# Kernel tuning notes

Measured on AMD Instinct MI355X. Metric: run time of the kernel, lower is better.

Reference implementation:

```python
import jax, jax.numpy as jnp
import numpy as np

B, H, S, D = 4, 16, 2048, 128
D_MODEL = 128  # scale factor per module init


def setup_inputs() -> dict:
    key = jax.random.key(0)
    kq, kk, kv = jax.random.split(key, 3)
    Q = jax.random.normal(kq, (B, H, S, D), dtype=jnp.float32)
    K = jax.random.normal(kk, (B, H, S, D), dtype=jnp.float32)
    V = jax.random.normal(kv, (B, H, S, D), dtype=jnp.float32)
    return {"Q": Q, "K": K, "V": V}


def reference(Q, K, V):
    # scores: [B, H, S, S]
    scores = jnp.einsum("bhqd,bhkd->bhqk", Q, K) / np.sqrt(D_MODEL).astype(np.float32)
    # causal mask: lower-triangular keeps, upper becomes -inf
    q_idx = jnp.arange(S)[:, None]
    k_idx = jnp.arange(S)[None, :]
    causal = q_idx >= k_idx  # [S, S]
    scores = jnp.where(causal, scores, -jnp.inf)
    attn = jax.nn.softmax(scores, axis=-1)
    return jnp.einsum("bhqk,bhkd->bhqd", attn, V)
```

## Files before the change

### kernel.cpp

```cpp
#include <hip/hip_runtime.h>

typedef _Float16 f16;
typedef _Float16 f16x8 __attribute__((ext_vector_type(8)));
typedef float    f32x16 __attribute__((ext_vector_type(16)));
typedef int      i32x4 __attribute__((ext_vector_type(4)));

#define B_ 4
#define H_ 16
#define S_ 2048
#define D_ 128
#define KVB 32
#define KSTR 136
#define VTSTR 40

union U4 { i32x4 i; f16x8 h; };

__device__ __forceinline__ unsigned pk2(float a, float b) {
    auto v = __builtin_amdgcn_cvt_pkrtz(a, b);
    return __builtin_bit_cast(unsigned, v);
}

__device__ __forceinline__ f16x8 cvt8(const float4 a, const float4 b) {
    f16x8 h;
    h[0] = (f16)a.x; h[1] = (f16)a.y; h[2] = (f16)a.z; h[3] = (f16)a.w;
    h[4] = (f16)b.x; h[5] = (f16)b.y; h[6] = (f16)b.z; h[7] = (f16)b.w;
    return h;
}

__global__ __launch_bounds__(256)
void prep(const float* __restrict__ K, const float* __restrict__ V,
          f16* __restrict__ Kh, f16* __restrict__ Vtt)
{
    const int bid = blockIdx.x;
    const int bh  = bid >> 5;
    const int kb  = bid & 31;
    const int k0  = kb * 64;
    const int tid = threadIdx.x;

    const float* Kb = K + ((size_t)bh * S_ + k0) * D_;
    const float* Vb = V + ((size_t)bh * S_ + k0) * D_;
    f16* Khb = Kh + ((size_t)bh * S_ + k0) * D_;
    f16* Vtb = Vtt + (size_t)bh * S_ * D_ + (size_t)kb * 2 * (D_ * 32);

    #pragma unroll
    for (int it = 0; it < 4; ++it) {
        const int idx = tid + it * 256;
        const int row = idx >> 4, c8 = idx & 15;
        const float4 a = *(const float4*)(Kb + row * D_ + c8 * 8);
        const float4 b = *(const float4*)(Kb + row * D_ + c8 * 8 + 4);
        *(f16x8*)(Khb + row * D_ + c8 * 8) = cvt8(a, b);
    }
    #pragma unroll
    for (int it = 0; it < 4; ++it) {
        const int idx = tid + it * 256;
        const int d  = idx & 127;
        const int k8 = idx >> 7;
        const int t  = k8 >> 2;
        const int o  = k8 & 3;
        const int c  = o >> 1, odd = o & 1;
        const int kbase = t * 32 + c * 16 + odd * 4;
        const float* vp0 = Vb + (size_t)kbase * D_ + d;
        const float* vp1 = vp0 + (size_t)8 * D_;
        f16x8 vh;
        #pragma unroll
        for (int e = 0; e < 4; ++e) vh[e] = (f16)vp0[(size_t)e * D_];
        #pragma unroll
        for (int e = 0; e < 4; ++e) vh[4 + e] = (f16)vp1[(size_t)e * D_];
        *(f16x8*)(Vtb + (size_t)t * (D_ * 32) + d * 32 + o * 8) = vh;
    }
}

__global__ __launch_bounds__(256, 2)
void fattn15(const float* __restrict__ Qg, const f16* __restrict__ Khg,
             const f16* __restrict__ Vttg, float* __restrict__ Og)
{
    __shared__ __align__(16) f16 Klds[4][KVB * KSTR];
    __shared__ __align__(16) f16 Vt[4][128 * VTSTR];

    const int id  = blockIdx.x;
    const int xcd = id & 7;
    const int r   = id >> 3;
    const int bh  = xcd + 8 * (r & 7);
    const int p   = r >> 3;

    const int tid  = threadIdx.x;
    const int lane = tid & 63;
    const int l31  = lane & 31;
    const int h    = lane >> 5;
    const int wv   = tid >> 6;

    const float* Qb  = Qg   + (size_t)bh * S_ * D_;
    const f16*   Khb = Khg  + (size_t)bh * S_ * D_;
    const f16*   Vtb = Vttg + (size_t)bh * S_ * D_;
    float*       Ob  = Og   + (size_t)bh * S_ * D_;

    const f16* kS = Khb + (tid >> 4) * D_ + (tid & 15) * 8;
    const f16* vS = Vtb + (size_t)tid * 8;
    const int  kDo = (tid >> 4) * KSTR + (tid & 15) * 8;
    const int  vDo = (tid >> 2) * VTSTR + (tid & 3) * 8;

    i32x4 kr[2], vr[2];
    auto issue = [&](int kt) {
        const f16* kp = kS + ((size_t)kt << 12);
        const f16* vp = vS + ((size_t)kt << 12);
        kr[0] = *(const i32x4*)kp;
        kr[1] = *(const i32x4*)(kp + 2048);
        vr[0] = *(const i32x4*)vp;
        vr[1] = *(const i32x4*)(vp + 2048);
    };
    auto writeLds = [&](int buf) {
        f16* kb = &Klds[buf][0];
        f16* vb = &Vt[buf][0];
        *(i32x4*)(kb + kDo)              = kr[0];
        *(i32x4*)(kb + kDo + 16 * KSTR)  = kr[1];
        *(i32x4*)(vb + vDo)              = vr[0];
        *(i32x4*)(vb + vDo + 64 * VTSTR) = vr[1];
    };
    f16x8 qf[8];
    auto qkt = [&](int buf) {
        f32x16 a;
        #pragma unroll
        for (int rr = 0; rr < 16; ++rr) a[rr] = 0.f;
        #pragma unroll
        for (int dc = 0; dc < 8; ++dc) {
            const f16x8 kf = *(const f16x8*)&Klds[buf][l31 * KSTR + dc * 16 + h * 8];
            a = __builtin_amdgcn_mfma_f32_32x32x16_f16(kf, qf[dc], a, 0, 0, 0);
        }
        return a;
    };

    const float qmul = 0.08838834764831845f * 1.4426950408889634f;

    #pragma unroll 1
    for (int ph = 0; ph < 2; ++ph) {
        const int qt  = ph ? 15 - p : p;
        const int qw0 = qt * 128 + wv * 32;
        const int qg  = qw0 + l31;
        const int nkt = 4 * qt + 4;
        const int lastt = 4 * qt + wv;

        {
            const float* Qrow = Qb + (size_t)(qw0 + l31) * D_;
            #pragma unroll
            for (int dc = 0; dc < 8; ++dc) {
                const float4 a = *(const float4*)(Qrow + dc * 16 + h * 8);
                const float4 b = *(const float4*)(Qrow + dc * 16 + h * 8 + 4);
                f16x8 q;
                q[0] = (f16)(a.x * qmul); q[1] = (f16)(a.y * qmul);
                q[2] = (f16)(a.z * qmul); q[3] = (f16)(a.w * qmul);
                q[4] = (f16)(b.x * qmul); q[5] = (f16)(b.y * qmul);
                q[6] = (f16)(b.z * qmul); q[7] = (f16)(b.w * qmul);
                qf[dc] = q;
            }
        }

        f32x16 acc[4];
        #pragma unroll
        for (int dt = 0; dt < 4; ++dt)
            #pragma unroll
            for (int rr = 0; rr < 16; ++rr) acc[dt][rr] = 0.f;
        float m_i = -1e30f, l_i = 0.f;

        __syncthreads();
        issue(0);  writeLds(0);
        issue(1);  writeLds(1);
        if (nkt > 2) issue(2);
        __syncthreads();
        f32x16 sv = qkt(0);

        U4 pa0c, pa1c, pa0p, pa1p;

        for (int kt = 0; kt < nkt; ++kt) {
            __syncthreads();
            if (kt + 2 < nkt) {
                writeLds((kt + 2) & 3);
                if (kt + 3 < nkt) issue(kt + 3);
            }

            __builtin_amdgcn_s_setprio(1);
            f32x16 svn;
            const bool doA = (kt + 1 < nkt) && (kt + 1 <= lastt);
            if (doA) svn = qkt((kt + 1) & 3);

            if (kt >= 1 && kt - 1 <= lastt) {
                const f16* vbase = &Vt[(kt - 1) & 3][l31 * VTSTR + h * 8];
                #pragma unroll
                for (int dt = 0; dt < 4; ++dt) {
                    const f16x8 vb0 = *(const f16x8*)(vbase + dt * 32 * VTSTR);
                    const f16x8 vb1 = *(const f16x8*)(vbase + dt * 32 * VTSTR + 16);
                    acc[dt] = __builtin_amdgcn_mfma_f32_32x32x16_f16(pa0p.h, vb0, acc[dt], 0, 0, 0);
                    acc[dt] = __builtin_amdgcn_mfma_f32_32x32x16_f16(pa1p.h, vb1, acc[dt], 0, 0, 0);
                }
            }

            if (kt <= lastt) {
                const int k0 = kt * KVB;
                if (k0 + 31 > qw0) {
                    #pragma unroll
                    for (int rr = 0; rr < 16; ++rr) {
                        const int kg = k0 + (rr & 3) + 8 * (rr >> 2) + 4 * h;
                        if (kg > qg) sv[rr] = -1e30f;
                    }
                }
                const float m1 = fmaxf(fmaxf(sv[0], sv[1]), sv[2]);
                const float m2 = fmaxf(fmaxf(sv[3], sv[4]), sv[5]);
                const float m3 = fmaxf(fmaxf(sv[6], sv[7]), sv[8]);
                const float m4 = fmaxf(fmaxf(sv[9], sv[10]), sv[11]);
                const float m5 = fmaxf(fmaxf(sv[12], sv[13]), sv[14]);
                float mx = fmaxf(fmaxf(m1, m2), m3);
                mx = fmaxf(fmaxf(mx, m4), m5);
                mx = fmaxf(mx, sv[15]);
                mx = fmaxf(mx, __shfl_xor(mx, 32));
                if (!__all(mx - m_i <= 8.0f)) {
                    const float mn = fmaxf(m_i, mx);
                    const float al = exp2f(m_i - mn);
                    m_i = mn;
                    l_i *= al;
                    float arow[16];
                    #pragma unroll
                    for (int rr = 0; rr < 16; ++rr)
                        arow[rr] = __shfl(al, (rr & 3) + 8 * (rr >> 2) + 4 * h);
                    #pragma unroll
                    for (int dt = 0; dt < 4; ++dt)
                        #pragma unroll
                        for (int rr = 0; rr < 16; ++rr) acc[dt][rr] *= arow[rr];
                }
                #pragma unroll
                for (int rr = 0; rr < 16; ++rr) sv[rr] = exp2f(sv[rr] - m_i);
                float s8[8];
                #pragma unroll
                for (int rr = 0; rr < 8; ++rr) s8[rr] = sv[2 * rr] + sv[2 * rr + 1];
                #pragma unroll
                for (int rr = 0; rr < 4; ++rr) s8[rr] += s8[rr + 4];
                s8[0] += s8[2]; s8[1] += s8[3];
                float rs = s8[0] + s8[1];
                rs += __shfl_xor(rs, 32);
                l_i += rs;
                #pragma unroll
                for (int m = 0; m < 4; ++m) pa0c.i[m] = (int)pk2(sv[2 * m],     sv[2 * m + 1]);
                #pragma unroll
                for (int m = 0; m < 4; ++m) pa1c.i[m] = (int)pk2(sv[8 + 2 * m], sv[9 + 2 * m]);
            }
            __builtin_amdgcn_s_setprio(0);

            pa0p = pa0c; pa1p = pa1c;
            if (doA) sv = svn;
        }

        if (lastt == nkt - 1) {
            const f16* vbase = &Vt[lastt & 3][l31 * VTSTR + h * 8];
            #pragma unroll
            for (int dt = 0; dt < 4; ++dt) {
                const f16x8 vb0 = *(const f16x8*)(vbase + dt * 32 * VTSTR);
                const f16x8 vb1 = *(const f16x8*)(vbase + dt * 32 * VTSTR + 16);
                acc[dt] = __builtin_amdgcn_mfma_f32_32x32x16_f16(pa0p.h, vb0, acc[dt], 0, 0, 0);
                acc[dt] = __builtin_amdgcn_mfma_f32_32x32x16_f16(pa1p.h, vb1, acc[dt], 0, 0, 0);
            }
        }

        float li[16];
        #pragma unroll
        for (int rr = 0; rr < 16; ++rr) {
            const float lv = __shfl(l_i, (rr & 3) + 8 * (rr >> 2) + 4 * h);
            li[rr] = 1.0f / lv;
        }
        #pragma unroll
        for (int dt = 0; dt < 4; ++dt)
            #pragma unroll
            for (int rr = 0; rr < 16; ++rr) {
                const int row = qw0 + (rr & 3) + 8 * (rr >> 2) + 4 * h;
                Ob[(size_t)row * D_ + dt * 32 + l31] = acc[dt][rr] * li[rr];
            }
    }
}

__global__ __launch_bounds__(256, 3)
void fattn5(const float* __restrict__ Qg, const float* __restrict__ Kg,
            const float* __restrict__ Vg, float* __restrict__ Og)
{
    __shared__ __align__(16) f16 Klds[2][KVB * KSTR];
    __shared__ __align__(16) f16 Vt[2][128 * VTSTR];
    const int id  = blockIdx.x;
    const int xcd = id & 7;
    const int w   = id >> 3;
    const int qt  = 15 - (w & 15);
    const int bh  = xcd + 8 * (w >> 4);
    const int tid  = threadIdx.x;
    const int lane = tid & 63;
    const int wv   = tid >> 6;
    const int l31  = lane & 31;
    const int h    = lane >> 5;
    const int qw0 = qt * 128 + wv * 32;
    const int qg  = qw0 + l31;
    const size_t base = (size_t)bh * S_ * D_;
    const float* Qb = Qg + base;
    const float* Kb = Kg + base;
    const float* Vb = Vg + base;
    float*       Ob = Og + base;
    const int nkt = 4 * qt + 4;
    float4 kr[4];
    float  vr[16];
    auto issue = [&](int kt) {
        const int k0n = kt * KVB;
        #pragma unroll
        for (int it = 0; it < 2; ++it) {
            const int idx  = tid + it * 256;
            const int krow = idx >> 4;
            const int c8   = idx & 15;
            const float* kp = Kb + (size_t)(k0n + krow) * D_ + c8 * 8;
            kr[it * 2]     = *(const float4*)kp;
            kr[it * 2 + 1] = *(const float4*)(kp + 4);
            const int d  = idx & 127;
            const int k8 = idx >> 7;
            const float* vp = Vb + (size_t)(k0n + k8 * 8) * D_ + d;
            #pragma unroll
            for (int e = 0; e < 8; ++e) vr[it * 8 + e] = vp[(size_t)e * D_];
        }
    };
    auto writeLds = [&](int buf) {
        #pragma unroll
        for (int it = 0; it < 2; ++it) {
            const int idx  = tid + it * 256;
            const int krow = idx >> 4;
            const int c8   = idx & 15;
            *(f16x8*)&Klds[buf][krow * KSTR + c8 * 8] = cvt8(kr[it * 2], kr[it * 2 + 1]);
            const int d  = idx & 127;
            const int k8 = idx >> 7;
            f16x8 vh;
            #pragma unroll
            for (int e = 0; e < 8; ++e) vh[e] = (f16)vr[it * 8 + e];
            *(f16x8*)&Vt[buf][d * VTSTR + k8 * 8] = vh;
        }
    };
    const float qmul = 0.08838834764831845f * 1.4426950408889634f;
    f16x8 qf[8];
    {
        const float* Qrow = Qb + (size_t)(qw0 + l31) * D_;
        #pragma unroll
        for (int dc = 0; dc < 8; ++dc) {
            const float4 a = *(const float4*)(Qrow + dc * 16 + h * 8);
            const float4 b = *(const float4*)(Qrow + dc * 16 + h * 8 + 4);
            f16x8 q;
            q[0] = (f16)(a.x * qmul); q[1] = (f16)(a.y * qmul);
            q[2] = (f16)(a.z * qmul); q[3] = (f16)(a.w * qmul);
            q[4] = (f16)(b.x * qmul); q[5] = (f16)(b.y * qmul);
            q[6] = (f16)(b.z * qmul); q[7] = (f16)(b.w * qmul);
            qf[dc] = q;
        }
    }
    f32x16 acc[4];
    #pragma unroll
    for (int dt = 0; dt < 4; ++dt)
        #pragma unroll
        for (int rr = 0; rr < 16; ++rr) acc[dt][rr] = 0.f;
    float m_i = -1e30f, l_i = 0.f;
    issue(0);
    writeLds(0);
    if (nkt > 1) issue(1);
    __syncthreads();
    for (int kt = 0; kt < nkt; ++kt) {
        const int k0  = kt * KVB;
        const int cur = kt & 1;
        if (k0 <= qw0 + 31) {
            f32x16 sv;
            #pragma unroll
            for (int rr = 0; rr < 16; ++rr) sv[rr] = 0.f;
            #pragma unroll
            for (int dc = 0; dc < 8; ++dc) {
                const f16x8 kf = *(const f16x8*)&Klds[cur][l31 * KSTR + dc * 16 + h * 8];
                sv = __builtin_amdgcn_mfma_f32_32x32x16_f16(kf, qf[dc], sv, 0, 0, 0);
            }
            if (k0 + 31 > qw0) {
                #pragma unroll
                for (int rr = 0; rr < 16; ++rr) {
                    const int kg = k0 + (rr & 3) + 8 * (rr >> 2) + 4 * h;
                    if (kg > qg) sv[rr] = -1e30f;
                }
            }
            float mx = sv[0];
            #pragma unroll
            for (int rr = 1; rr < 16; ++rr) mx = fmaxf(mx, sv[rr]);
            mx = fmaxf(mx, __shfl_xor(mx, 32));
            if (!__all(mx - m_i <= 8.0f)) {
                const float mn = fmaxf(m_i, mx);
                const float al = exp2f(m_i - mn);
                m_i = mn;
                l_i *= al;
                float arow[16];
                #pragma unroll
                for (int rr = 0; rr < 16; ++rr)
                    arow[rr] = __shfl(al, (rr & 3) + 8 * (rr >> 2) + 4 * h);
                #pragma unroll
                for (int dt = 0; dt < 4; ++dt)
                    #pragma unroll
                    for (int rr = 0; rr < 16; ++rr) acc[dt][rr] *= arow[rr];
            }
            float rs = 0.f;
            #pragma unroll
            for (int rr = 0; rr < 16; ++rr) {
                sv[rr] = exp2f(sv[rr] - m_i);
                rs += sv[rr];
            }
            rs += __shfl_xor(rs, 32);
            l_i += rs;
            U4 pa[2];
            {
                unsigned dwp[8];
                #pragma unroll
                for (int m = 0; m < 8; ++m) dwp[m] = pk2(sv[2 * m], sv[2 * m + 1]);
                #pragma unroll
                for (int hf = 0; hf < 2; ++hf) {
                    const unsigned a0 = dwp[hf * 4 + 0], a1 = dwp[hf * 4 + 1];
                    const unsigned b0 = dwp[hf * 4 + 2], b1 = dwp[hf * 4 + 3];
                    const unsigned sa0 = (unsigned)__shfl_xor((int)a0, 32);
                    const unsigned sa1 = (unsigned)__shfl_xor((int)a1, 32);
                    const unsigned sb0 = (unsigned)__shfl_xor((int)b0, 32);
                    const unsigned sb1 = (unsigned)__shfl_xor((int)b1, 32);
                    i32x4 d;
                    d[0] = h ? (int)sb0 : (int)a0;
                    d[1] = h ? (int)sb1 : (int)a1;
                    d[2] = h ? (int)b0  : (int)sa0;
                    d[3] = h ? (int)b1  : (int)sa1;
                    pa[hf].i = d;
                }
            }
            #pragma unroll
            for (int dt = 0; dt < 4; ++dt) {
                const f16* vrow = &Vt[cur][(dt * 32 + l31) * VTSTR + h * 8];
                const f16x8 vb0 = *(const f16x8*)(vrow + 0);
                const f16x8 vb1 = *(const f16x8*)(vrow + 16);
                acc[dt] = __builtin_amdgcn_mfma_f32_32x32x16_f16(pa[0].h, vb0, acc[dt], 0, 0, 0);
                acc[dt] = __builtin_amdgcn_mfma_f32_32x32x16_f16(pa[1].h, vb1, acc[dt], 0, 0, 0);
            }
        }
        if (kt + 1 < nkt) {
            writeLds(cur ^ 1);
            if (kt + 2 < nkt) issue(kt + 2);
            __syncthreads();
        }
    }
    float li[16];
    #pragma unroll
    for (int rr = 0; rr < 16; ++rr) {
        const float lv = __shfl(l_i, (rr & 3) + 8 * (rr >> 2) + 4 * h);
        li[rr] = 1.0f / lv;
    }
    #pragma unroll
    for (int dt = 0; dt < 4; ++dt)
        #pragma unroll
        for (int rr = 0; rr < 16; ++rr) {
            const int row = qw0 + (rr & 3) + 8 * (rr >> 2) + 4 * h;
            Ob[(size_t)row * D_ + dt * 32 + l31] = acc[dt][rr] * li[rr];
        }
}

extern "C" void kernel_launch(void* const* d_in, const int* in_sizes, int n_in,
                              void* d_out, int out_size, void* d_ws, size_t ws_size,
                              hipStream_t stream) {
    (void)in_sizes; (void)n_in; (void)out_size;
    const float* Q = (const float*)d_in[0];
    const float* K = (const float*)d_in[1];
    const float* V = (const float*)d_in[2];
    float* O = (float*)d_out;
    const size_t elems  = (size_t)B_ * H_ * S_ * D_;
    const size_t needKV = elems * 2 * sizeof(f16);
    if (ws_size >= needKV) {
        f16* Kh  = (f16*)d_ws;
        f16* Vtt = Kh + elems;
        prep<<<dim3(B_ * H_ * (S_ / 64)), dim3(256), 0, stream>>>(K, V, Kh, Vtt);
        fattn15<<<dim3(512), dim3(256), 0, stream>>>(Q, Kh, Vtt, O);
    } else {
        fattn5<<<dim3((S_ / 128) * B_ * H_), dim3(256), 0, stream>>>(Q, K, V, O);
    }
}
```

Measured before the change: 156.0 us.

## Use 64-key tiles with double buffering instead of 4-stage software-pipelined 32-key tiles

Doubles the KV tile to 64 keys and drops from four LDS buffers to two. It also removes the software pipelining that overlapped the next tile's QK^T with the current PV, and instead computes two 32-key score blocks per iteration in sequence. This halves the number of barriers and iterations and raises MFMA work per sync. In exchange it loses the cross-iteration overlap and coarsens causal skipping, so wasted masked work grows on diagonal tiles.

Result: no change. 156.3 us (+0.2%).

```diff
diff --git a/kernel.cpp b/kernel.cpp
--- a/kernel.cpp
+++ b/kernel.cpp
@@ -9,9 +9,9 @@
 #define H_ 16
 #define S_ 2048
 #define D_ 128
-#define KVB 32
+#define KVB 64
 #define KSTR 136
-#define VTSTR 40
+#define VT2  72
 
 union U4 { i32x4 i; f16x8 h; };
 
@@ -71,11 +71,11 @@
 }
 
 __global__ __launch_bounds__(256, 2)
-void fattn15(const float* __restrict__ Qg, const f16* __restrict__ Khg,
+void fattn16(const float* __restrict__ Qg, const f16* __restrict__ Khg,
              const f16* __restrict__ Vttg, float* __restrict__ Og)
 {
-    __shared__ __align__(16) f16 Klds[4][KVB * KSTR];
-    __shared__ __align__(16) f16 Vt[4][128 * VTSTR];
+    __shared__ __align__(16) f16 Klds[2][KVB * KSTR];
+    __shared__ __align__(16) f16 Vl[2][128 * VT2];
 
     const int id  = blockIdx.x;
     const int xcd = id & 7;
@@ -97,37 +97,31 @@
     const f16* kS = Khb + (tid >> 4) * D_ + (tid & 15) * 8;
     const f16* vS = Vtb + (size_t)tid * 8;
     const int  kDo = (tid >> 4) * KSTR + (tid & 15) * 8;
-    const int  vDo = (tid >> 2) * VTSTR + (tid & 3) * 8;
-
-    i32x4 kr[2], vr[2];
+    const int  vDo = (tid >> 2) * VT2 + (tid & 3) * 8;
+
+    i32x4 kr[4], vr[4];
     auto issue = [&](int kt) {
-        const f16* kp = kS + ((size_t)kt << 12);
-        const f16* vp = vS + ((size_t)kt << 12);
-        kr[0] = *(const i32x4*)kp;
-        kr[1] = *(const i32x4*)(kp + 2048);
-        vr[0] = *(const i32x4*)vp;
-        vr[1] = *(const i32x4*)(vp + 2048);
+        const f16* kp = kS + ((size_t)kt << 13);
+        const f16* vp = vS + ((size_t)kt << 13);
+        #pragma unroll
+        for (int it = 0; it < 4; ++it) {
+            kr[it] = *(const i32x4*)(kp + it * 2048);
+            vr[it] = *(const i32x4*)(vp + it * 2048);
+        }
     };
     auto writeLds = [&](int buf) {
         f16* kb = &Klds[buf][0];
-        f16* vb = &Vt[buf][0];
+        f16* vb = &Vl[buf][0];
         *(i32x4*)(kb + kDo)              = kr[0];
         *(i32x4*)(kb + kDo + 16 * KSTR)  = kr[1];
+        *(i32x4*)(kb + kDo + 32 * KSTR)  = kr[2];
+        *(i32x4*)(kb + kDo + 48 * KSTR)  = kr[3];
         *(i32x4*)(vb + vDo)              = vr[0];
-        *(i32x4*)(vb + vDo + 64 * VTSTR) = vr[1];
+        *(i32x4*)(vb + vDo + 64 * VT2)   = vr[1];
+        *(i32x4*)(vb + vDo + 32)         = vr[2];
+        *(i32x4*)(vb + vDo + 64 * VT2 + 32) = vr[3];
     };
     f16x8 qf[8];
-    auto qkt = [&](int buf) {
-        f32x16 a;
-        #pragma unroll
-        for (int rr = 0; rr < 16; ++rr) a[rr] = 0.f;
-        #pragma unroll
-        for (int dc = 0; dc < 8; ++dc) {
-            const f16x8 kf = *(const f16x8*)&Klds[buf][l31 * KSTR + dc * 16 + h * 8];
-            a = __builtin_amdgcn_mfma_f32_32x32x16_f16(kf, qf[dc], a, 0, 0, 0);
-        }
-        return a;
-    };
 
     const float qmul = 0.08838834764831845f * 1.4426950408889634f;
 
@@ -136,9 +130,10 @@
         const int qt  = ph ? 15 - p : p;
         const int qw0 = qt * 128 + wv * 32;
         const int qg  = qw0 + l31;
-        const int nkt = 4 * qt + 4;
-        const int lastt = 4 * qt + wv;
-
+        const int nt  = 2 * qt + 2;
+        const int lastt = (4 * qt + wv) >> 1;
+
+        issue(0);
         {
             const float* Qrow = Qb + (size_t)(qw0 + l31) * D_;
             #pragma unroll
@@ -162,54 +157,43 @@
         float m_i = -1e30f, l_i = 0.f;
 
         __syncthreads();
-        issue(0);  writeLds(0);
-        issue(1);  writeLds(1);
-        if (nkt > 2) issue(2);
+        writeLds(0);
+        if (nt > 1) issue(1);
         __syncthreads();
-        f32x16 sv = qkt(0);
-
-        U4 pa0c, pa1c, pa0p, pa1p;
-
-        for (int kt = 0; kt < nkt; ++kt) {
-            __syncthreads();
-            if (kt + 2 < nkt) {
-                writeLds((kt + 2) & 3);
-                if (kt + 3 < nkt) issue(kt + 3);
-            }
-
-            __builtin_amdgcn_s_setprio(1);
-            f32x16 svn;
-            const bool doA = (kt + 1 < nkt) && (kt + 1 <= lastt);
-            if (doA) svn = qkt((kt + 1) & 3);
-
-            if (kt >= 1 && kt - 1 <= lastt) {
-                const f16* vbase = &Vt[(kt - 1) & 3][l31 * VTSTR + h * 8];
-                #pragma unroll
-                for (int dt = 0; dt < 4; ++dt) {
-                    const f16x8 vb0 = *(const f16x8*)(vbase + dt * 32 * VTSTR);
-                    const f16x8 vb1 = *(const f16x8*)(vbase + dt * 32 * VTSTR + 16);
-                    acc[dt] = __builtin_amdgcn_mfma_f32_32x32x16_f16(pa0p.h, vb0, acc[dt], 0, 0, 0);
-                    acc[dt] = __builtin_amdgcn_mfma_f32_32x32x16_f16(pa1p.h, vb1, acc[dt], 0, 0, 0);
-                }
-            }
+
+        for (int kt = 0; kt < nt; ++kt) {
+            const int cur = kt & 1;
 
             if (kt <= lastt) {
                 const int k0 = kt * KVB;
-                if (k0 + 31 > qw0) {
+                f32x16 sv0, sv1;
+                #pragma unroll
+                for (int rr = 0; rr < 16; ++rr) { sv0[rr] = 0.f; sv1[rr] = 0.f; }
+                __builtin_amdgcn_s_setprio(1);
+                #pragma unroll
+                for (int dc = 0; dc < 8; ++dc) {
+                    const f16x8 kf0 = *(const f16x8*)&Klds[cur][l31 * KSTR + dc * 16 + h * 8];
+                    const f16x8 kf1 = *(const f16x8*)&Klds[cur][(32 + l31) * KSTR + dc * 16 + h * 8];
+                    sv0 = __builtin_amdgcn_mfma_f32_32x32x16_f16(kf0, qf[dc], sv0, 0, 0, 0);
+                    sv1 = __builtin_amdgcn_mfma_f32_32x32x16_f16(kf1, qf[dc], sv1, 0, 0, 0);
+                }
+                __builtin_amdgcn_s_setprio(0);
+                if (k0 + 63 > qw0) {
                     #pragma unroll
                     for (int rr = 0; rr < 16; ++rr) {
-                        const int kg = k0 + (rr & 3) + 8 * (rr >> 2) + 4 * h;
-                        if (kg > qg) sv[rr] = -1e30f;
+                        const int kk = k0 + (rr & 3) + 8 * (rr >> 2) + 4 * h;
+                        if (kk > qg)      sv0[rr] = -1e30f;
+                        if (kk + 32 > qg) sv1[rr] = -1e30f;
                     }
                 }
-                const float m1 = fmaxf(fmaxf(sv[0], sv[1]), sv[2]);
-                const float m2 = fmaxf(fmaxf(sv[3], sv[4]), sv[5]);
-                const float m3 = fmaxf(fmaxf(sv[6], sv[7]), sv[8]);
-                const float m4 = fmaxf(fmaxf(sv[9], sv[10]), sv[11]);
-                const float m5 = fmaxf(fmaxf(sv[12], sv[13]), sv[14]);
-                float mx = fmaxf(fmaxf(m1, m2), m3);
-                mx = fmaxf(fmaxf(mx, m4), m5);
-                mx = fmaxf(mx, sv[15]);
+                float t16[16];
+                #pragma unroll
+                for (int rr = 0; rr < 16; ++rr) t16[rr] = fmaxf(sv0[rr], sv1[rr]);
+                #pragma unroll
+                for (int rr = 0; rr < 8; ++rr) t16[rr] = fmaxf(t16[rr], t16[rr + 8]);
+                #pragma unroll
+                for (int rr = 0; rr < 4; ++rr) t16[rr] = fmaxf(t16[rr], t16[rr + 4]);
+                float mx = fmaxf(fmaxf(t16[0], t16[1]), fmaxf(t16[2], t16[3]));
                 mx = fmaxf(mx, __shfl_xor(mx, 32));
                 if (!__all(mx - m_i <= 8.0f)) {
                     const float mn = fmaxf(m_i, mx);
@@ -226,35 +210,48 @@
                         for (int rr = 0; rr < 16; ++rr) acc[dt][rr] *= arow[rr];
                 }
                 #pragma unroll
-                for (int rr = 0; rr < 16; ++rr) sv[rr] = exp2f(sv[rr] - m_i);
-                float s8[8];
-                #pragma unroll
-                for (int rr = 0; rr < 8; ++rr) s8[rr] = sv[2 * rr] + sv[2 * rr + 1];
-                #pragma unroll
-                for (int rr = 0; rr < 4; ++rr) s8[rr] += s8[rr + 4];
-                s8[0] += s8[2]; s8[1] += s8[3];
-                float rs = s8[0] + s8[1];
+                for (int rr = 0; rr < 16; ++rr) {
+                    sv0[rr] = exp2f(sv0[rr] - m_i);
+                    sv1[rr] = exp2f(sv1[rr] - m_i);
+                }
+                float s16[16];
+                #pragma unroll
+                for (int rr = 0; rr < 16; ++rr) s16[rr] = sv0[rr] + sv1[rr];
+                #pragma unroll
+                for (int rr = 0; rr < 8; ++rr) s16[rr] += s16[rr + 8];
+                #pragma unroll
+                for (int rr = 0; rr < 4; ++rr) s16[rr] += s16[rr + 4];
+                float rs = (s16[0] + s16[1]) + (s16[2] + s16[3]);
                 rs += __shfl_xor(rs, 32);
                 l_i += rs;
-                #pragma unroll
-                for (int m = 0; m < 4; ++m) pa0c.i[m] = (int)pk2(sv[2 * m],     sv[2 * m + 1]);
-                #pragma unroll
-                for (int m = 0; m < 4; ++m) pa1c.i[m] = (int)pk2(sv[8 + 2 * m], sv[9 + 2 * m]);
-            }
-            __builtin_amdgcn_s_setprio(0);
-
-            pa0p = pa0c; pa1p = pa1c;
-            if (doA) sv = svn;
-        }
-
-        if (lastt == nkt - 1) {
-            const f16* vbase = &Vt[lastt & 3][l31 * VTSTR + h * 8];
-            #pragma unroll
-            for (int dt = 0; dt < 4; ++dt) {
-                const f16x8 vb0 = *(const f16x8*)(vbase + dt * 32 * VTSTR);
-                const f16x8 vb1 = *(const f16x8*)(vbase + dt * 32 * VTSTR + 16);
-                acc[dt] = __builtin_amdgcn_mfma_f32_32x32x16_f16(pa0p.h, vb0, acc[dt], 0, 0, 0);
-                acc[dt] = __builtin_amdgcn_mfma_f32_32x32x16_f16(pa1p.h, vb1, acc[dt], 0, 0, 0);
+                U4 pa[4];
+                #pragma unroll
+                for (int m = 0; m < 4; ++m) {
+                    pa[0].i[m] = (int)pk2(sv0[2 * m],     sv0[2 * m + 1]);
+                    pa[1].i[m] = (int)pk2(sv0[8 + 2 * m], sv0[9 + 2 * m]);
+                    pa[2].i[m] = (int)pk2(sv1[2 * m],     sv1[2 * m + 1]);
+                    pa[3].i[m] = (int)pk2(sv1[8 + 2 * m], sv1[9 + 2 * m]);
+                }
+                __builtin_amdgcn_s_setprio(1);
+                #pragma unroll
+                for (int dt = 0; dt < 4; ++dt) {
+                    const f16* vrow = &Vl[cur][(dt * 32 + l31) * VT2 + h * 8];
+                    const f16x8 b0 = *(const f16x8*)(vrow + 0);
+                    const f16x8 b1 = *(const f16x8*)(vrow + 16);
+                    const f16x8 b2 = *(const f16x8*)(vrow + 32);
+                    const f16x8 b3 = *(const f16x8*)(vrow + 48);
+                    acc[dt] = __builtin_amdgcn_mfma_f32_32x32x16_f16(pa[0].h, b0, acc[dt], 0, 0, 0);
+                    acc[dt] = __builtin_amdgcn_mfma_f32_32x32x16_f16(pa[1].h, b1, acc[dt], 0, 0, 0);
+                    acc[dt] = __builtin_amdgcn_mfma_f32_32x32x16_f16(pa[2].h, b2, acc[dt], 0, 0, 0);
+                    acc[dt] = __builtin_amdgcn_mfma_f32_32x32x16_f16(pa[3].h, b3, acc[dt], 0, 0, 0);
+                }
+                __builtin_amdgcn_s_setprio(0);
+            }
+
+            if (kt + 1 < nt) {
+                writeLds(cur ^ 1);
+                if (kt + 2 < nt) issue(kt + 2);
+                __syncthreads();
             }
         }
 
@@ -274,12 +271,14 @@
     }
 }
 
+#define KVB5 32
+#define VTSTR5 40
 __global__ __launch_bounds__(256, 3)
 void fattn5(const float* __restrict__ Qg, const float* __restrict__ Kg,
             const float* __restrict__ Vg, float* __restrict__ Og)
 {
-    __shared__ __align__(16) f16 Klds[2][KVB * KSTR];
-    __shared__ __align__(16) f16 Vt[2][128 * VTSTR];
+    __shared__ __align__(16) f16 Klds[2][KVB5 * KSTR];
+    __shared__ __align__(16) f16 Vt[2][128 * VTSTR5];
     const int id  = blockIdx.x;
     const int xcd = id & 7;
     const int w   = id >> 3;
@@ -301,7 +300,7 @@
     float4 kr[4];
     float  vr[16];
     auto issue = [&](int kt) {
-        const int k0n = kt * KVB;
+        const int k0n = kt * KVB5;
         #pragma unroll
         for (int it = 0; it < 2; ++it) {
             const int idx  = tid + it * 256;
@@ -329,7 +328,7 @@
             f16x8 vh;
             #pragma unroll
             for (int e = 0; e < 8; ++e) vh[e] = (f16)vr[it * 8 + e];
-            *(f16x8*)&Vt[buf][d * VTSTR + k8 * 8] = vh;
+            *(f16x8*)&Vt[buf][d * VTSTR5 + k8 * 8] = vh;
         }
     };
     const float qmul = 0.08838834764831845f * 1.4426950408889634f;
@@ -359,7 +358,7 @@
     if (nkt > 1) issue(1);
     __syncthreads();
     for (int kt = 0; kt < nkt; ++kt) {
-        const int k0  = kt * KVB;
+        const int k0  = kt * KVB5;
         const int cur = kt & 1;
         if (k0 <= qw0 + 31) {
             f32x16 sv;
@@ -426,7 +425,7 @@
             }
             #pragma unroll
             for (int dt = 0; dt < 4; ++dt) {
-                const f16* vrow = &Vt[cur][(dt * 32 + l31) * VTSTR + h * 8];
+                const f16* vrow = &Vt[cur][(dt * 32 + l31) * VTSTR5 + h * 8];
                 const f16x8 vb0 = *(const f16x8*)(vrow + 0);
                 const f16x8 vb1 = *(const f16x8*)(vrow + 16);
                 acc[dt] = __builtin_amdgcn_mfma_f32_32x32x16_f16(pa[0].h, vb0, acc[dt], 0, 0, 0);
@@ -468,7 +467,7 @@
         f16* Kh  = (f16*)d_ws;
         f16* Vtt = Kh + elems;
         prep<<<dim3(B_ * H_ * (S_ / 64)), dim3(256), 0, stream>>>(K, V, Kh, Vtt);
-        fattn15<<<dim3(512), dim3(256), 0, stream>>>(Q, Kh, Vtt, O);
+        fattn16<<<dim3(512), dim3(256), 0, stream>>>(Q, Kh, Vtt, O);
     } else {
         fattn5<<<dim3((S_ / 128) * B_ * H_), dim3(256), 0, stream>>>(Q, K, V, O);
     }
```

## Split causal KV range into two halves with partial outputs and merge kernel

Applied to the files above, without the earlier changes.

Replaces the paired-qtile persistent attention kernel with a split-K style design. Each query tile is processed by two blocks covering the lower and upper halves of the causal KV range, which write f16 partial outputs plus per-row (m, l) to workspace; a separate merge kernel combines them. Q is also pre-scaled and converted to f16 in the prep kernel, and LDS buffering drops from four to two stages to allow three blocks per CU. This raises parallelism and occupancy, at the cost of extra global traffic for partials, a third launch, f16 rounding of partial outputs, and loss of the software-pipelined QK/PV overlap.

Measured after the change: 185.7 us. 1.19x slower.

```diff
diff --git a/kernel.cpp b/kernel.cpp
--- a/kernel.cpp
+++ b/kernel.cpp
@@ -1,6 +1,7 @@
 #include <hip/hip_runtime.h>
 
 typedef _Float16 f16;
+typedef _Float16 f16x4 __attribute__((ext_vector_type(4)));
 typedef _Float16 f16x8 __attribute__((ext_vector_type(8)));
 typedef float    f32x16 __attribute__((ext_vector_type(16)));
 typedef int      i32x4 __attribute__((ext_vector_type(4)));
@@ -29,17 +30,21 @@
 
 __global__ __launch_bounds__(256)
 void prep(const float* __restrict__ K, const float* __restrict__ V,
-          f16* __restrict__ Kh, f16* __restrict__ Vtt)
+          const float* __restrict__ Q,
+          f16* __restrict__ Kh, f16* __restrict__ Vtt, f16* __restrict__ Qh)
 {
     const int bid = blockIdx.x;
     const int bh  = bid >> 5;
     const int kb  = bid & 31;
     const int k0  = kb * 64;
     const int tid = threadIdx.x;
+    const float qmul = 0.08838834764831845f * 1.4426950408889634f;
 
     const float* Kb = K + ((size_t)bh * S_ + k0) * D_;
     const float* Vb = V + ((size_t)bh * S_ + k0) * D_;
+    const float* Qb = Q + ((size_t)bh * S_ + k0) * D_;
     f16* Khb = Kh + ((size_t)bh * S_ + k0) * D_;
+    f16* Qhb = Qh + ((size_t)bh * S_ + k0) * D_;
     f16* Vtb = Vtt + (size_t)bh * S_ * D_ + (size_t)kb * 2 * (D_ * 32);
 
     #pragma unroll
@@ -49,6 +54,11 @@
         const float4 a = *(const float4*)(Kb + row * D_ + c8 * 8);
         const float4 b = *(const float4*)(Kb + row * D_ + c8 * 8 + 4);
         *(f16x8*)(Khb + row * D_ + c8 * 8) = cvt8(a, b);
+        float4 qa = *(const float4*)(Qb + row * D_ + c8 * 8);
+        float4 qb = *(const float4*)(Qb + row * D_ + c8 * 8 + 4);
+        qa.x *= qmul; qa.y *= qmul; qa.z *= qmul; qa.w *= qmul;
+        qb.x *= qmul; qb.y *= qmul; qb.z *= qmul; qb.w *= qmul;
+        *(f16x8*)(Qhb + row * D_ + c8 * 8) = cvt8(qa, qb);
     }
     #pragma unroll
     for (int it = 0; it < 4; ++it) {
@@ -70,18 +80,21 @@
     }
 }
 
-__global__ __launch_bounds__(256, 2)
-void fattn15(const float* __restrict__ Qg, const f16* __restrict__ Khg,
-             const f16* __restrict__ Vttg, float* __restrict__ Og)
+__global__ __launch_bounds__(256, 3)
+void fattn17(const f16* __restrict__ Qhg, const f16* __restrict__ Khg,
+             const f16* __restrict__ Vttg,
+             f16* __restrict__ Pg, float2* __restrict__ mlg)
 {
-    __shared__ __align__(16) f16 Klds[4][KVB * KSTR];
-    __shared__ __align__(16) f16 Vt[4][128 * VTSTR];
+    __shared__ __align__(16) f16 Klds[2][KVB * KSTR];
+    __shared__ __align__(16) f16 Vl[2][128 * VTSTR];
 
     const int id  = blockIdx.x;
     const int xcd = id & 7;
     const int r   = id >> 3;
     const int bh  = xcd + 8 * (r & 7);
-    const int p   = r >> 3;
+    const int rr  = r >> 3;
+    const int s   = rr & 1;
+    const int qt  = 15 - (rr >> 1);
 
     const int tid  = threadIdx.x;
     const int lane = tid & 63;
@@ -89,10 +102,19 @@
     const int h    = lane >> 5;
     const int wv   = tid >> 6;
 
-    const float* Qb  = Qg   + (size_t)bh * S_ * D_;
-    const f16*   Khb = Khg  + (size_t)bh * S_ * D_;
-    const f16*   Vtb = Vttg + (size_t)bh * S_ * D_;
-    float*       Ob  = Og   + (size_t)bh * S_ * D_;
+    const int qw0 = qt * 128 + wv * 32;
+    const int qg  = qw0 + l31;
+
+    const f16* Qhb = Qhg + (size_t)bh * S_ * D_;
+    const f16* Khb = Khg + (size_t)bh * S_ * D_;
+    const f16* Vtb = Vttg + (size_t)bh * S_ * D_;
+
+    const int nkt  = 4 * qt + 4;
+    const int half = 2 * qt + 2;
+    const int lo   = s ? half : 0;
+    const int hi   = s ? nkt : half;
+    int lastt = 4 * qt + wv;
+    if (lastt > hi - 1) lastt = hi - 1;
 
     const f16* kS = Khb + (tid >> 4) * D_ + (tid & 15) * 8;
     const f16* vS = Vtb + (size_t)tid * 8;
@@ -110,167 +132,156 @@
     };
     auto writeLds = [&](int buf) {
         f16* kb = &Klds[buf][0];
-        f16* vb = &Vt[buf][0];
+        f16* vb = &Vl[buf][0];
         *(i32x4*)(kb + kDo)              = kr[0];
         *(i32x4*)(kb + kDo + 16 * KSTR)  = kr[1];
         *(i32x4*)(vb + vDo)              = vr[0];
         *(i32x4*)(vb + vDo + 64 * VTSTR) = vr[1];
     };
+
     f16x8 qf[8];
-    auto qkt = [&](int buf) {
-        f32x16 a;
-        #pragma unroll
-        for (int rr = 0; rr < 16; ++rr) a[rr] = 0.f;
-        #pragma unroll
-        for (int dc = 0; dc < 8; ++dc) {
-            const f16x8 kf = *(const f16x8*)&Klds[buf][l31 * KSTR + dc * 16 + h * 8];
-            a = __builtin_amdgcn_mfma_f32_32x32x16_f16(kf, qf[dc], a, 0, 0, 0);
-        }
-        return a;
-    };
-
-    const float qmul = 0.08838834764831845f * 1.4426950408889634f;
-
-    #pragma unroll 1
-    for (int ph = 0; ph < 2; ++ph) {
-        const int qt  = ph ? 15 - p : p;
-        const int qw0 = qt * 128 + wv * 32;
-        const int qg  = qw0 + l31;
-        const int nkt = 4 * qt + 4;
-        const int lastt = 4 * qt + wv;
-
-        {
-            const float* Qrow = Qb + (size_t)(qw0 + l31) * D_;
+    {
+        const f16* Qrow = Qhb + (size_t)(qw0 + l31) * D_;
+        #pragma unroll
+        for (int dc = 0; dc < 8; ++dc)
+            qf[dc] = *(const f16x8*)(Qrow + dc * 16 + h * 8);
+    }
+
+    f32x16 acc[4];
+    #pragma unroll
+    for (int dt = 0; dt < 4; ++dt)
+        #pragma unroll
+        for (int q = 0; q < 16; ++q) acc[dt][q] = 0.f;
+    float m_i = -1e30f, l_i = 0.f;
+
+    issue(lo);
+    writeLds(0);
+    if (lo + 1 < hi) issue(lo + 1);
+    __syncthreads();
+
+    for (int kt = lo; kt < hi; ++kt) {
+        const int cur = (kt - lo) & 1;
+
+        if (kt <= lastt) {
+            const int k0 = kt * KVB;
+            f32x16 sv;
+            #pragma unroll
+            for (int q = 0; q < 16; ++q) sv[q] = 0.f;
+            __builtin_amdgcn_s_setprio(1);
             #pragma unroll
             for (int dc = 0; dc < 8; ++dc) {
-                const float4 a = *(const float4*)(Qrow + dc * 16 + h * 8);
-                const float4 b = *(const float4*)(Qrow + dc * 16 + h * 8 + 4);
-                f16x8 q;
-                q[0] = (f16)(a.x * qmul); q[1] = (f16)(a.y * qmul);
-                q[2] = (f16)(a.z * qmul); q[3] = (f16)(a.w * qmul);
-                q[4] = (f16)(b.x * qmul); q[5] = (f16)(b.y * qmul);
-                q[6] = (f16)(b.z * qmul); q[7] = (f16)(b.w * qmul);
-                qf[dc] = q;
-            }
-        }
-
-        f32x16 acc[4];
-        #pragma unroll
-        for (int dt = 0; dt < 4; ++dt)
-            #pragma unroll
-            for (int rr = 0; rr < 16; ++rr) acc[dt][rr] = 0.f;
-        float m_i = -1e30f, l_i = 0.f;
-
-        __syncthreads();
-        issue(0);  writeLds(0);
-        issue(1);  writeLds(1);
-        if (nkt > 2) issue(2);
-        __syncthreads();
-        f32x16 sv = qkt(0);
-
-        U4 pa0c, pa1c, pa0p, pa1p;
-
-        for (int kt = 0; kt < nkt; ++kt) {
+                const f16x8 kf = *(const f16x8*)&Klds[cur][l31 * KSTR + dc * 16 + h * 8];
+                sv = __builtin_amdgcn_mfma_f32_32x32x16_f16(kf, qf[dc], sv, 0, 0, 0);
+            }
+            __builtin_amdgcn_s_setprio(0);
+            if (k0 + 31 > qw0) {
+                #pragma unroll
+                for (int q = 0; q < 16; ++q) {
+                    const int kg = k0 + (q & 3) + 8 * (q >> 2) + 4 * h;
+                    if (kg > qg) sv[q] = -1e30f;
+                }
+            }
+            const float a1 = fmaxf(fmaxf(sv[0], sv[1]), sv[2]);
+            const float a2 = fmaxf(fmaxf(sv[3], sv[4]), sv[5]);
+            const float a3 = fmaxf(fmaxf(sv[6], sv[7]), sv[8]);
+            const float a4 = fmaxf(fmaxf(sv[9], sv[10]), sv[11]);
+            const float a5 = fmaxf(fmaxf(sv[12], sv[13]), sv[14]);
+            float mx = fmaxf(fmaxf(a1, a2), a3);
+            mx = fmaxf(fmaxf(mx, a4), a5);
+            mx = fmaxf(mx, sv[15]);
+            mx = fmaxf(mx, __shfl_xor(mx, 32));
+            if (!__all(mx - m_i <= 8.0f)) {
+                const float mn = fmaxf(m_i, mx);
+                const float al = exp2f(m_i - mn);
+                m_i = mn;
+                l_i *= al;
+                float arow[16];
+                #pragma unroll
+                for (int q = 0; q < 16; ++q)
+                    arow[q] = __shfl(al, (q & 3) + 8 * (q >> 2) + 4 * h);
+                #pragma unroll
+                for (int dt = 0; dt < 4; ++dt)
+                    #pragma unroll
+                    for (int q = 0; q < 16; ++q) acc[dt][q] *= arow[q];
+            }
+            #pragma unroll
+            for (int q = 0; q < 16; ++q) sv[q] = exp2f(sv[q] - m_i);
+            float s8[8];
+            #pragma unroll
+            for (int q = 0; q < 8; ++q) s8[q] = sv[2 * q] + sv[2 * q + 1];
+            #pragma unroll
+            for (int q = 0; q < 4; ++q) s8[q] += s8[q + 4];
+            s8[0] += s8[2]; s8[1] += s8[3];
+            float rsum = s8[0] + s8[1];
+            rsum += __shfl_xor(rsum, 32);
+            l_i += rsum;
+            U4 pa0, pa1;
+            #pragma unroll
+            for (int m = 0; m < 4; ++m) {
+                pa0.i[m] = (int)pk2(sv[2 * m],     sv[2 * m + 1]);
+                pa1.i[m] = (int)pk2(sv[8 + 2 * m], sv[9 + 2 * m]);
+            }
+            __builtin_amdgcn_s_setprio(1);
+            #pragma unroll
+            for (int dt = 0; dt < 4; ++dt) {
+                const f16* vrow = &Vl[cur][(dt * 32 + l31) * VTSTR + h * 8];
+                const f16x8 b0 = *(const f16x8*)(vrow + 0);
+                const f16x8 b1 = *(const f16x8*)(vrow + 16);
+                acc[dt] = __builtin_amdgcn_mfma_f32_32x32x16_f16(pa0.h, b0, acc[dt], 0, 0, 0);
+                acc[dt] = __builtin_amdgcn_mfma_f32_32x32x16_f16(pa1.h, b1, acc[dt], 0, 0, 0);
+            }
+            __builtin_amdgcn_s_setprio(0);
+        }
+
+        if (kt + 1 < hi) {
+            writeLds(cur ^ 1);
+            if (kt + 2 < hi) issue(kt + 2);
             __syncthreads();
-            if (kt + 2 < nkt) {
-                writeLds((kt + 2) & 3);
-                if (kt + 3 < nkt) issue(kt + 3);
-            }
-
-            __builtin_amdgcn_s_setprio(1);
-            f32x16 svn;
-            const bool doA = (kt + 1 < nkt) && (kt + 1 <= lastt);
-            if (doA) svn = qkt((kt + 1) & 3);
-
-            if (kt >= 1 && kt - 1 <= lastt) {
-                const f16* vbase = &Vt[(kt - 1) & 3][l31 * VTSTR + h * 8];
-                #pragma unroll
-                for (int dt = 0; dt < 4; ++dt) {
-                    const f16x8 vb0 = *(const f16x8*)(vbase + dt * 32 * VTSTR);
-                    const f16x8 vb1 = *(const f16x8*)(vbase + dt * 32 * VTSTR + 16);
-                    acc[dt] = __builtin_amdgcn_mfma_f32_32x32x16_f16(pa0p.h, vb0, acc[dt], 0, 0, 0);
-                    acc[dt] = __builtin_amdgcn_mfma_f32_32x32x16_f16(pa1p.h, vb1, acc[dt], 0, 0, 0);
-                }
-            }
-
-            if (kt <= lastt) {
-                const int k0 = kt * KVB;
-                if (k0 + 31 > qw0) {
-                    #pragma unroll
-                    for (int rr = 0; rr < 16; ++rr) {
-                        const int kg = k0 + (rr & 3) + 8 * (rr >> 2) + 4 * h;
-                        if (kg > qg) sv[rr] = -1e30f;
-                    }
-                }
-                const float m1 = fmaxf(fmaxf(sv[0], sv[1]), sv[2]);
-                const float m2 = fmaxf(fmaxf(sv[3], sv[4]), sv[5]);
-                const float m3 = fmaxf(fmaxf(sv[6], sv[7]), sv[8]);
-                const float m4 = fmaxf(fmaxf(sv[9], sv[10]), sv[11]);
-                const float m5 = fmaxf(fmaxf(sv[12], sv[13]), sv[14]);
-                float mx = fmaxf(fmaxf(m1, m2), m3);
-                mx = fmaxf(fmaxf(mx, m4), m5);
-                mx = fmaxf(mx, sv[15]);
-                mx = fmaxf(mx, __shfl_xor(mx, 32));
-                if (!__all(mx - m_i <= 8.0f)) {
-                    const float mn = fmaxf(m_i, mx);
-                    const float al = exp2f(m_i - mn);
-                    m_i = mn;
-                    l_i *= al;
-                    float arow[16];
-                    #pragma unroll
-                    for (int rr = 0; rr < 16; ++rr)
-                        arow[rr] = __shfl(al, (rr & 3) + 8 * (rr >> 2) + 4 * h);
-                    #pragma unroll
-                    for (int dt = 0; dt < 4; ++dt)
-                        #pragma unroll
-                        for (int rr = 0; rr < 16; ++rr) acc[dt][rr] *= arow[rr];
-                }
-                #pragma unroll
-                for (int rr = 0; rr < 16; ++rr) sv[rr] = exp2f(sv[rr] - m_i);
-                float s8[8];
-                #pragma unroll
-                for (int rr = 0; rr < 8; ++rr) s8[rr] = sv[2 * rr] + sv[2 * rr + 1];
-                #pragma unroll
-                for (int rr = 0; rr < 4; ++rr) s8[rr] += s8[rr + 4];
-                s8[0] += s8[2]; s8[1] += s8[3];
-                float rs = s8[0] + s8[1];
-                rs += __shfl_xor(rs, 32);
-                l_i += rs;
-                #pragma unroll
-                for (int m = 0; m < 4; ++m) pa0c.i[m] = (int)pk2(sv[2 * m],     sv[2 * m + 1]);
-                #pragma unroll
-                for (int m = 0; m < 4; ++m) pa1c.i[m] = (int)pk2(sv[8 + 2 * m], sv[9 + 2 * m]);
-            }
-            __builtin_amdgcn_s_setprio(0);
-
-            pa0p = pa0c; pa1p = pa1c;
-            if (doA) sv = svn;
-        }
-
-        if (lastt == nkt - 1) {
-            const f16* vbase = &Vt[lastt & 3][l31 * VTSTR + h * 8];
-            #pragma unroll
-            for (int dt = 0; dt < 4; ++dt) {
-                const f16x8 vb0 = *(const f16x8*)(vbase + dt * 32 * VTSTR);
-                const f16x8 vb1 = *(const f16x8*)(vbase + dt * 32 * VTSTR + 16);
-                acc[dt] = __builtin_amdgcn_mfma_f32_32x32x16_f16(pa0p.h, vb0, acc[dt], 0, 0, 0);
-                acc[dt] = __builtin_amdgcn_mfma_f32_32x32x16_f16(pa1p.h, vb1, acc[dt], 0, 0, 0);
-            }
-        }
-
-        float li[16];
-        #pragma unroll
-        for (int rr = 0; rr < 16; ++rr) {
-            const float lv = __shfl(l_i, (rr & 3) + 8 * (rr >> 2) + 4 * h);
-            li[rr] = 1.0f / lv;
-        }
-        #pragma unroll
-        for (int dt = 0; dt < 4; ++dt)
-            #pragma unroll
-            for (int rr = 0; rr < 16; ++rr) {
-                const int row = qw0 + (rr & 3) + 8 * (rr >> 2) + 4 * h;
-                Ob[(size_t)row * D_ + dt * 32 + l31] = acc[dt][rr] * li[rr];
-            }
+        }
+    }
+
+    float li[16];
+    #pragma unroll
+    for (int q = 0; q < 16; ++q) {
+        const float lv = __shfl(l_i, (q & 3) + 8 * (q >> 2) + 4 * h);
+        li[q] = (lv > 0.f) ? 1.0f / lv : 0.f;
+    }
+    f16* Pb = Pg + ((size_t)s * (B_ * H_) + bh) * (S_ * D_);
+    #pragma unroll
+    for (int dt = 0; dt < 4; ++dt)
+        #pragma unroll
+        for (int q = 0; q < 16; ++q) {
+            const int row = qw0 + (q & 3) + 8 * (q >> 2) + 4 * h;
+            Pb[(size_t)row * D_ + dt * 32 + l31] = (f16)(acc[dt][q] * li[q]);
+        }
+    if (h == 0)
+        mlg[((size_t)s * (B_ * H_) + bh) * S_ + qw0 + l31] = make_float2(m_i, l_i);
+}
+
+__global__ __launch_bounds__(256)
+void merge(const f16* __restrict__ Pg, const float2* __restrict__ mlg,
+           float* __restrict__ O)
+{
+    const size_t NROW   = (size_t)B_ * H_ * S_;
+    const size_t total4 = NROW * (D_ / 4);
+    const size_t stride = (size_t)gridDim.x * 256;
+    for (size_t i = (size_t)blockIdx.x * 256 + threadIdx.x; i < total4; i += stride) {
+        const size_t row = i >> 5;
+        const float2 a = mlg[row];
+        const float2 b = mlg[NROW + row];
+        const float ms = fmaxf(a.x, b.x);
+        float w0 = exp2f(a.x - ms) * a.y;
+        float w1 = exp2f(b.x - ms) * b.y;
+        const float inv = 1.0f / (w0 + w1);
+        w0 *= inv; w1 *= inv;
+        const f16x4 p0 = *(const f16x4*)(Pg + i * 4);
+        const f16x4 p1 = *(const f16x4*)(Pg + NROW * D_ + i * 4);
+        float4 o;
+        o.x = w0 * (float)p0[0] + w1 * (float)p1[0];
+        o.y = w0 * (float)p0[1] + w1 * (float)p1[1];
+        o.z = w0 * (float)p0[2] + w1 * (float)p1[2];
+        o.w = w0 * (float)p0[3] + w1 * (float)p1[3];
+        *(float4*)(O + i * 4) = o;
     }
 }
 
@@ -352,7 +363,7 @@
     #pragma unroll
     for (int dt = 0; dt < 4; ++dt)
         #pragma unroll
-        for (int rr = 0; rr < 16; ++rr) acc[dt][rr] = 0.f;
+        for (int q = 0; q < 16; ++q) acc[dt][q] = 0.f;
     float m_i = -1e30f, l_i = 0.f;
     issue(0);
     writeLds(0);
@@ -364,7 +375,7 @@
         if (k0 <= qw0 + 31) {
             f32x16 sv;
             #pragma unroll
-            for (int rr = 0; rr < 16; ++rr) sv[rr] = 0.f;
+            for (int q = 0; q < 16; ++q) sv[q] = 0.f;
             #pragma unroll
             for (int dc = 0; dc < 8; ++dc) {
                 const f16x8 kf = *(const f16x8*)&Klds[cur][l31 * KSTR + dc * 16 + h * 8];
@@ -372,14 +383,14 @@
             }
             if (k0 + 31 > qw0) {
                 #pragma unroll
-                for (int rr = 0; rr < 16; ++rr) {
-                    const int kg = k0 + (rr & 3) + 8 * (rr >> 2) + 4 * h;
-                    if (kg > qg) sv[rr] = -1e30f;
+                for (int q = 0; q < 16; ++q) {
+                    const int kg = k0 + (q & 3) + 8 * (q >> 2) + 4 * h;
+                    if (kg > qg) sv[q] = -1e30f;
                 }
             }
             float mx = sv[0];
             #pragma unroll
-            for (int rr = 1; rr < 16; ++rr) mx = fmaxf(mx, sv[rr]);
+            for (int q = 1; q < 16; ++q) mx = fmaxf(mx, sv[q]);
             mx = fmaxf(mx, __shfl_xor(mx, 32));
             if (!__all(mx - m_i <= 8.0f)) {
                 const float mn = fmaxf(m_i, mx);
@@ -388,21 +399,21 @@
                 l_i *= al;
                 float arow[16];
                 #pragma unroll
-                for (int rr = 0; rr < 16; ++rr)
-                    arow[rr] = __shfl(al, (rr & 3) + 8 * (rr >> 2) + 4 * h);
+                for (int q = 0; q < 16; ++q)
+                    arow[q] = __shfl(al, (q & 3) + 8 * (q >> 2) + 4 * h);
                 #pragma unroll
                 for (int dt = 0; dt < 4; ++dt)
                     #pragma unroll
-                    for (int rr = 0; rr < 16; ++rr) acc[dt][rr] *= arow[rr];
-            }
-            float rs = 0.f;
-            #pragma unroll
-            for (int rr = 0; rr < 16; ++rr) {
-                sv[rr] = exp2f(sv[rr] - m_i);
-                rs += sv[rr];
-            }
-            rs += __shfl_xor(rs, 32);
-            l_i += rs;
+                    for (int q = 0; q < 16; ++q) acc[dt][q] *= arow[q];
+            }
+            float rsum = 0.f;
+            #pragma unroll
+            for (int q = 0; q < 16; ++q) {
+                sv[q] = exp2f(sv[q] - m_i);
+                rsum += sv[q];
+            }
+            rsum += __shfl_xor(rsum, 32);
+            l_i += rsum;
             U4 pa[2];
             {
                 unsigned dwp[8];
@@ -441,16 +452,16 @@
     }
     float li[16];
     #pragma unroll
-    for (int rr = 0; rr < 16; ++rr) {
-        const float lv = __shfl(l_i, (rr & 3) + 8 * (rr >> 2) + 4 * h);
-        li[rr] = 1.0f / lv;
+    for (int q = 0; q < 16; ++q) {
+        const float lv = __shfl(l_i, (q & 3) + 8 * (q >> 2) + 4 * h);
+        li[q] = 1.0f / lv;
     }
     #pragma unroll
     for (int dt = 0; dt < 4; ++dt)
         #pragma unroll
-        for (int rr = 0; rr < 16; ++rr) {
-            const int row = qw0 + (rr & 3) + 8 * (rr >> 2) + 4 * h;
-            Ob[(size_t)row * D_ + dt * 32 + l31] = acc[dt][rr] * li[rr];
+        for (int q = 0; q < 16; ++q) {
+            const int row = qw0 + (q & 3) + 8 * (q >> 2) + 4 * h;
+            Ob[(size_t)row * D_ + dt * 32 + l31] = acc[dt][q] * li[q];
         }
 }
 
@@ -462,13 +473,18 @@
     const float* K = (const float*)d_in[1];
     const float* V = (const float*)d_in[2];
     float* O = (float*)d_out;
-    const size_t elems  = (size_t)B_ * H_ * S_ * D_;
-    const size_t needKV = elems * 2 * sizeof(f16);
-    if (ws_size >= needKV) {
+    const size_t elems = (size_t)B_ * H_ * S_ * D_;
+    const size_t nrow  = (size_t)B_ * H_ * S_;
+    const size_t need  = elems * 2 * 5 + nrow * sizeof(float2) * 2;
+    if (ws_size >= need) {
         f16* Kh  = (f16*)d_ws;
         f16* Vtt = Kh + elems;
-        prep<<<dim3(B_ * H_ * (S_ / 64)), dim3(256), 0, stream>>>(K, V, Kh, Vtt);
-        fattn15<<<dim3(512), dim3(256), 0, stream>>>(Q, Kh, Vtt, O);
+        f16* Qh  = Vtt + elems;
+        f16* P   = Qh + elems;
+        float2* ml = (float2*)(P + 2 * elems);
+        prep<<<dim3(B_ * H_ * (S_ / 64)), dim3(256), 0, stream>>>(K, V, Q, Kh, Vtt, Qh);
+        fattn17<<<dim3(2048), dim3(256), 0, stream>>>(Qh, Kh, Vtt, P, ml);
+        merge<<<dim3(2048), dim3(256), 0, stream>>>(P, ml, O);
     } else {
         fattn5<<<dim3((S_ / 128) * B_ * H_), dim3(256), 0, stream>>>(Q, K, V, O);
     }
```
